# Performance work log

Measured on AMD Instinct MI355X. Metric: run time of the kernel, lower is better.

Reference implementation:

```python
import jax, jax.numpy as jnp
import numpy as np

EPS_BN = 1e-5
EPS_NORM = 1e-12
NUM_HEADS = 8


def _bn_relu(x):
    # BatchNorm2d in training mode with fresh params (gamma=1, beta=0), then ReLU.
    m = x.mean((0, 2, 3), keepdims=True)
    v = x.var((0, 2, 3), keepdims=True)  # biased variance, as PyTorch uses for normalization
    return jax.nn.relu((x - m) * jax.lax.rsqrt(v + EPS_BN))


def _conv3(x, w, groups=1):
    # 3x3 conv, stride 1, padding 1 (NCHW / OIHW)
    return jax.lax.conv_general_dilated(
        x, w, (1, 1), ((1, 1), (1, 1)),
        dimension_numbers=('NCHW', 'OIHW', 'NCHW'),
        feature_group_count=groups)


def _encoder(x, w1, w2, w3):
    # Conv1x1 -> BN -> ReLU -> Conv k2 s2 -> BN -> ReLU -> Conv1x1 -> BN -> ReLU
    x = _bn_relu(jnp.einsum('bihw,oi->bohw', x, w1))
    b, c, h, w = x.shape
    # k=2,s=2 conv as a reshape + einsum (non-overlapping 2x2 patches)
    x = _bn_relu(jnp.einsum('bchpwq,ocpq->bohw', x.reshape(b, c, h // 2, 2, w // 2, 2), w2))
    return _bn_relu(jnp.einsum('bihw,oi->bohw', x, w3))


def _decoder(x, w1, w2, w3):
    # ConvT1x1 -> BN -> ReLU -> ConvT k2 s2 -> BN -> ReLU -> ConvT1x1 -> BN -> ReLU
    x = _bn_relu(jnp.einsum('bihw,io->bohw', x, w1))
    # ConvTranspose k=2,s=2: each input pixel expands to a 2x2 block
    y = jnp.einsum('bihw,iopq->bohpwq', x, w2)
    b, o, h, p, w, q = y.shape
    x = _bn_relu(y.reshape(b, o, h * p, w * q))
    return _bn_relu(jnp.einsum('bihw,io->bohw', x, w3))


def _l2norm(x):
    # F.normalize(dim=-1) with eps=1e-12
    return x / jnp.maximum(jnp.linalg.norm(x, axis=-1, keepdims=True), EPS_NORM)


def setup_inputs() -> dict:
    key = jax.random.key(0)
    ks = jax.random.split(key, 13)
    B, C, H, W = 8, 256, 64, 64
    d = C // 4  # attention dim after self.divide

    def rn(k, shape, s=0.1):
        return jax.random.normal(k, shape, jnp.float32) * s

    return {
        'x': jax.random.normal(ks[0], (B, C, H, W), jnp.float32),
        'y': jax.random.normal(ks[1], (B, C, H, W), jnp.float32),
        'temperature': jnp.ones((NUM_HEADS, 1, 1), jnp.float32),
        'enc_w1': rn(ks[2], (d // 2, C)),
        'enc_w2': rn(ks[3], (d // 2, d // 2, 2, 2)),
        'enc_w3': rn(ks[4], (d, d // 2)),
        'kv_w': rn(ks[5], (2 * d, d)),
        'kv_dw_w': rn(ks[6], (2 * d, 1, 3, 3)),
        'q_w': rn(ks[7], (d, d)),
        'q_dw_w': rn(ks[8], (d, d, 3, 3)),
        'proj_w': rn(ks[9], (d, d)),
        'dec_w1': rn(ks[10], (d, 2 * d)),
        'dec_w2': rn(ks[11], (2 * d, 2 * d, 2, 2)),
        'dec_w3': rn(ks[12], (2 * d, 4 * d)),
    }


def reference(x, y, temperature, enc_w1, enc_w2, enc_w3, kv_w, kv_dw_w,
              q_w, q_dw_w, proj_w, dec_w1, dec_w2, dec_w3):
    # Shared freshly-built encoder applied to both x and y (same weights,
    # BN batch stats computed per call).
    x = _encoder(x, enc_w1, enc_w2, enc_w3)
    y = _encoder(y, enc_w1, enc_w2, enc_w3)
    b, c, h, w = x.shape  # c = 64, h = w = 32

    kv = _conv3(jnp.einsum('bihw,oi->bohw', x, kv_w), kv_dw_w, groups=2 * c)
    k, v = jnp.split(kv, 2, axis=1)
    q = _conv3(jnp.einsum('bihw,oi->bohw', y, q_w), q_dw_w)  # regular 3x3 conv

    ch = c // NUM_HEADS
    heads = lambda t: t.reshape(b, NUM_HEADS, ch, h * w)  # b head c (h w)
    q, k, v = heads(q), heads(k), heads(v)
    q = _l2norm(q)
    k = _l2norm(k)
    temp = temperature[None]  # [1, head, 1, 1]

    # Spatial attention: [b, head, hw, hw]
    attn_s = jax.nn.softmax(jnp.einsum('bhcn,bhcm->bhnm', q, k) * temp, axis=-1)
    out_s = jnp.einsum('bhcn,bhnm->bhcm', v, attn_s).reshape(b, c, h, w)
    out_s = jnp.einsum('bihw,oi->bohw', out_s, proj_w)

    # Channel attention: [b, head, c, c]
    attn_c = jax.nn.softmax(jnp.einsum('bhcn,bhdn->bhcd', q, k) * temp, axis=-1)
    out_c = jnp.einsum('bhcd,bhdn->bhcn', attn_c, v).reshape(b, c, h, w)
    out_c = jnp.einsum('bihw,oi->bohw', out_c, proj_w)

    return _decoder(out_s + out_c, dec_w1, dec_w2, dec_w3)
```

## Files before the change

### kernel.cpp

```cpp
#include <hip/hip_runtime.h>
#include <hip/hip_bf16.h>

#define EPS_BN 1e-5f

__global__ __launch_bounds__(256) void conv1x1_enc1_kernel(
    const float* __restrict__ in0, const float* __restrict__ in1,
    const float* __restrict__ w, float* __restrict__ out,
    float* __restrict__ stOut)
{
  __shared__ float il[2][32*64];
  __shared__ float wt[2][32*34];
  int tid  = threadIdx.x;
  int tile = blockIdx.x;
  int z    = blockIdx.y;
  int t    = z >> 3;
  const float* in  = t ? in1 : in0;
  const float* inb = in + ((size_t)(z&7))*256*4096 + tile*64;
  int cg = tid & 15;
  int og = tid >> 4;

  float4 vr[2]; float wr[4];
  int chA = tid >> 4;
  int chB = 16 + chA;
  int wo  = tid >> 5;
  int wch = tid & 31;

  vr[0] = *(const float4*)(inb + (size_t)chA*4096 + cg*4);
  vr[1] = *(const float4*)(inb + (size_t)chB*4096 + cg*4);
#pragma unroll
  for(int u=0;u<4;u++) wr[u] = w[(size_t)(wo+u*8)*256 + wch];
  ((float4*)il[0])[tid]     = vr[0];
  ((float4*)il[0])[tid+256] = vr[1];
#pragma unroll
  for(int u=0;u<4;u++) wt[0][wch*34 + wo + u*8] = wr[u];
  __syncthreads();

  float acc[2][4];
#pragma unroll
  for(int j=0;j<2;j++){ acc[j][0]=acc[j][1]=acc[j][2]=acc[j][3]=0.f; }

  for(int c=0;c<8;c++){
    int cur = c & 1;
    if(c < 7){
      int k0 = (c+1)*32;
      vr[0] = *(const float4*)(inb + (size_t)(k0+chA)*4096 + cg*4);
      vr[1] = *(const float4*)(inb + (size_t)(k0+chB)*4096 + cg*4);
#pragma unroll
      for(int u=0;u<4;u++) wr[u] = w[(size_t)(wo+u*8)*256 + k0 + wch];
    }
    const float4* ilc = (const float4*)il[cur];
    const float*  wtc = wt[cur];
#pragma unroll 8
    for(int ch=0; ch<32; ch++){
      float4 v  = ilc[ch*16 + cg];
      float2 wv = *(const float2*)&wtc[ch*34 + og*2];
      acc[0][0]=fmaf(wv.x,v.x,acc[0][0]); acc[0][1]=fmaf(wv.x,v.y,acc[0][1]);
      acc[0][2]=fmaf(wv.x,v.z,acc[0][2]); acc[0][3]=fmaf(wv.x,v.w,acc[0][3]);
      acc[1][0]=fmaf(wv.y,v.x,acc[1][0]); acc[1][1]=fmaf(wv.y,v.y,acc[1][1]);
      acc[1][2]=fmaf(wv.y,v.z,acc[1][2]); acc[1][3]=fmaf(wv.y,v.w,acc[1][3]);
    }
    if(c < 7){
      int nxt = 1 - cur;
      ((float4*)il[nxt])[tid]     = vr[0];
      ((float4*)il[nxt])[tid+256] = vr[1];
#pragma unroll
      for(int u=0;u<4;u++) wt[nxt][wch*34 + wo + u*8] = wr[u];
      __syncthreads();
    }
  }

  float* ob = out + ((size_t)z*32 + og*2)*4096 + tile*64 + cg*4;
#pragma unroll
  for(int j=0;j<2;j++){
    float4 vv = {acc[j][0],acc[j][1],acc[j][2],acc[j][3]};
    *(float4*)(ob + (size_t)j*4096) = vv;
  }
#pragma unroll
  for(int j=0;j<2;j++){
    float s  = acc[j][0]+acc[j][1]+acc[j][2]+acc[j][3];
    float s2 = acc[j][0]*acc[j][0]+acc[j][1]*acc[j][1]
             + acc[j][2]*acc[j][2]+acc[j][3]*acc[j][3];
    for(int off=8; off>0; off>>=1){
      s  += __shfl_down(s,  off, 16);
      s2 += __shfl_down(s2, off, 16);
    }
    if(cg==0){
      atomicAdd(&stOut[((size_t)t*32 + og*2 + j)*2],   s);
      atomicAdd(&stOut[((size_t)t*32 + og*2 + j)*2+1], s2);
    }
  }
}

template<int OT, bool HASBN, bool HASSTATS>
__global__ __launch_bounds__(256) void conv1x1_kernel(
    const float* __restrict__ in0, const float* __restrict__ in1,
    const float* __restrict__ w, float* __restrict__ out,
    const float* __restrict__ stIn, float* __restrict__ stOut,
    int I, int O, int P, int wio, int zsplit, float invN)
{
  __shared__ float wl[2048];
  __shared__ float bnm[256], bnr[256];
  int tid = threadIdx.x;
  int o0 = blockIdx.y*OT;
  int z  = blockIdx.z;
  int t  = (z >= zsplit) ? 1 : 0;
  int b  = t ? (z - zsplit) : z;
  const float* in = t ? in1 : in0;

  for(int idx=tid; idx<I*OT; idx+=256){
    int i = idx/OT, j = idx - i*OT;
    wl[idx] = wio ? w[(size_t)i*O + o0 + j] : w[(size_t)(o0+j)*I + i];
  }
  if(HASBN){
    for(int i=tid; i<I; i+=256){
      float s  = stIn[((size_t)t*I + i)*2];
      float s2 = stIn[((size_t)t*I + i)*2+1];
      float m  = s*invN;
      bnm[i] = m;
      bnr[i] = rsqrtf(s2*invN - m*m + EPS_BN);
    }
  }
  __syncthreads();

  int p4 = blockIdx.x*256 + tid;
  const float4* inb = (const float4*)(in + (size_t)b*I*P) + p4;
  int P4 = P >> 2;

  float acc[OT][4];
#pragma unroll
  for(int j=0;j<OT;j++){ acc[j][0]=acc[j][1]=acc[j][2]=acc[j][3]=0.f; }

  float4 vb[8];
  for(int i0=0;i0<I;i0+=8){
#pragma unroll
    for(int u=0;u<8;u++) vb[u] = inb[(size_t)(i0+u)*P4];
#pragma unroll
    for(int u=0;u<8;u++){
      float4 v = vb[u];
      if(HASBN){
        float m = bnm[i0+u], r = bnr[i0+u];
        v.x = fmaxf((v.x-m)*r, 0.f); v.y = fmaxf((v.y-m)*r, 0.f);
        v.z = fmaxf((v.z-m)*r, 0.f); v.w = fmaxf((v.w-m)*r, 0.f);
      }
      const float* wr = &wl[(i0+u)*OT];
#pragma unroll
      for(int j=0;j<OT;j++){
        float wv = wr[j];
        acc[j][0] = fmaf(wv, v.x, acc[j][0]);
        acc[j][1] = fmaf(wv, v.y, acc[j][1]);
        acc[j][2] = fmaf(wv, v.z, acc[j][2]);
        acc[j][3] = fmaf(wv, v.w, acc[j][3]);
      }
    }
  }

  float4* ob = (float4*)(out + ((size_t)z*O + o0)*P) + p4;
#pragma unroll
  for(int j=0;j<OT;j++){
    float4 vv = {acc[j][0], acc[j][1], acc[j][2], acc[j][3]};
    ob[(size_t)j*P4] = vv;
  }

  if(HASSTATS){
#pragma unroll
    for(int j=0;j<OT;j++){
      float s  = acc[j][0]+acc[j][1]+acc[j][2]+acc[j][3];
      float s2 = acc[j][0]*acc[j][0]+acc[j][1]*acc[j][1]
               + acc[j][2]*acc[j][2]+acc[j][3]*acc[j][3];
      for(int off=32; off>0; off>>=1){
        s  += __shfl_down(s,  off, 64);
        s2 += __shfl_down(s2, off, 64);
      }
      if((tid & 63)==0){
        atomicAdd(&stOut[((size_t)t*O + o0 + j)*2],   s);
        atomicAdd(&stOut[((size_t)t*O + o0 + j)*2+1], s2);
      }
    }
  }
}

template<int OT, bool HASBN, bool HASSTATS>
__global__ __launch_bounds__(256) void conv1x1_small(
    const float* __restrict__ in0, const float* __restrict__ in1,
    const float* __restrict__ w, float* __restrict__ out,
    const float* __restrict__ stIn, float* __restrict__ stOut,
    int I, int O, int wio, int zsplit, float invN)
{
  __shared__ float wl[512];
  __shared__ float bnm[128], bnr[128];
  int tid = threadIdx.x;
  int z  = blockIdx.z;
  int t  = (z >= zsplit) ? 1 : 0;
  int b  = t ? (z - zsplit) : z;
  const float* in = t ? in1 : in0;
  int W2 = 2*OT;

  for(int idx=tid; idx<I*W2; idx+=256){
    int i = idx/W2, slot = idx - i*W2;
    int oabs = blockIdx.y*W2 + slot;
    wl[idx] = wio ? w[(size_t)i*O + oabs] : w[(size_t)oabs*I + i];
  }
  if(HASBN){
    for(int i=tid; i<I; i+=256){
      float s  = stIn[((size_t)t*I + i)*2];
      float s2 = stIn[((size_t)t*I + i)*2+1];
      float m  = s*invN;
      bnm[i] = m;
      bnr[i] = rsqrtf(s2*invN - m*m + EPS_BN);
    }
  }
  __syncthreads();

  int p4 = blockIdx.x*128 + (tid & 127);
  int os = tid >> 7;
  const float4* inb = (const float4*)(in + (size_t)b*I*1024) + p4;

  float acc[OT][4];
#pragma unroll
  for(int j=0;j<OT;j++){ acc[j][0]=acc[j][1]=acc[j][2]=acc[j][3]=0.f; }

  float4 vb[8];
  for(int i0=0;i0<I;i0+=8){
#pragma unroll
    for(int u=0;u<8;u++) vb[u] = inb[(size_t)(i0+u)*256];
#pragma unroll
    for(int u=0;u<8;u++){
      float4 v = vb[u];
      if(HASBN){
        float m = bnm[i0+u], r = bnr[i0+u];
        v.x = fmaxf((v.x-m)*r, 0.f); v.y = fmaxf((v.y-m)*r, 0.f);
        v.z = fmaxf((v.z-m)*r, 0.f); v.w = fmaxf((v.w-m)*r, 0.f);
      }
      const float* wr = &wl[(i0+u)*W2 + os*OT];
#pragma unroll
      for(int j=0;j<OT;j++){
        float wv = wr[j];
        acc[j][0] = fmaf(wv, v.x, acc[j][0]);
        acc[j][1] = fmaf(wv, v.y, acc[j][1]);
        acc[j][2] = fmaf(wv, v.z, acc[j][2]);
        acc[j][3] = fmaf(wv, v.w, acc[j][3]);
      }
    }
  }

  int obase = blockIdx.y*W2 + os*OT;
  float4* ob = (float4*)(out + ((size_t)z*O + obase)*1024) + p4;
#pragma unroll
  for(int j=0;j<OT;j++){
    float4 vv = {acc[j][0], acc[j][1], acc[j][2], acc[j][3]};
    ob[(size_t)j*256] = vv;
  }

  if(HASSTATS){
#pragma unroll
    for(int j=0;j<OT;j++){
      float s  = acc[j][0]+acc[j][1]+acc[j][2]+acc[j][3];
      float s2 = acc[j][0]*acc[j][0]+acc[j][1]*acc[j][1]
               + acc[j][2]*acc[j][2]+acc[j][3]*acc[j][3];
      for(int off=32; off>0; off>>=1){
        s  += __shfl_down(s,  off, 64);
        s2 += __shfl_down(s2, off, 64);
      }
      if((tid & 63)==0){
        atomicAdd(&stOut[((size_t)t*O + obase + j)*2],   s);
        atomicAdd(&stOut[((size_t)t*O + obase + j)*2+1], s2);
      }
    }
  }
}

__global__ __launch_bounds__(256) void conv2x2s2_bn_kernel(
    const float* __restrict__ in, const float* __restrict__ w,
    float* __restrict__ out, const float* __restrict__ stIn,
    float* __restrict__ stOut, float invN)
{
  __shared__ float wl[512];
  __shared__ float bnm[32], bnr[32];
  int tid = threadIdx.x;
  int o0 = blockIdx.x*4;
  int rq = blockIdx.y;
  int z  = blockIdx.z;
  int t  = z >> 3;

  for(int idx=tid; idx<512; idx+=256){
    int osub = idx>>7, ch=(idx>>2)&31, pq=idx&3;
    wl[idx] = w[(((size_t)(o0+osub)*32 + ch)*4) + pq];
  }
  if(tid < 32){
    float s  = stIn[((size_t)t*32 + tid)*2];
    float s2 = stIn[((size_t)t*32 + tid)*2+1];
    float m  = s*invN;
    bnm[tid] = m;
    bnr[tid] = rsqrtf(s2*invN - m*m + EPS_BN);
  }
  __syncthreads();

  int os   = tid >> 6;
  int slot = tid & 63;
  int h    = rq*8 + (slot>>3);
  int wg   = slot & 7;
  int cb   = wg*8;
  const float* wbase = &wl[os*128];
  const float* inz = in + (size_t)z*32*4096;

  float acc[4] = {0,0,0,0};
  float4 c0,c1,c2,c3, n0_,n1_,n2_,n3_;
  c0 = *(const float4*)(inz + (size_t)0*4096 + (2*h)*64 + cb);
  c1 = *(const float4*)(inz + (size_t)0*4096 + (2*h)*64 + cb + 4);
  c2 = *(const float4*)(inz + (size_t)0*4096 + (2*h+1)*64 + cb);
  c3 = *(const float4*)(inz + (size_t)0*4096 + (2*h+1)*64 + cb + 4);
  for(int ch=0; ch<32; ch++){
    if(ch < 31){
      n0_ = *(const float4*)(inz + (size_t)(ch+1)*4096 + (2*h)*64 + cb);
      n1_ = *(const float4*)(inz + (size_t)(ch+1)*4096 + (2*h)*64 + cb + 4);
      n2_ = *(const float4*)(inz + (size_t)(ch+1)*4096 + (2*h+1)*64 + cb);
      n3_ = *(const float4*)(inz + (size_t)(ch+1)*4096 + (2*h+1)*64 + cb + 4);
    }
    float m = bnm[ch], r = bnr[ch];
    float t0[8] = {c0.x,c0.y,c0.z,c0.w,c1.x,c1.y,c1.z,c1.w};
    float t1[8] = {c2.x,c2.y,c2.z,c2.w,c3.x,c3.y,c3.z,c3.w};
#pragma unroll
    for(int e=0;e<8;e++){
      t0[e] = fmaxf((t0[e]-m)*r, 0.f);
      t1[e] = fmaxf((t1[e]-m)*r, 0.f);
    }
    const float* wp = wbase + ch*4;
#pragma unroll
    for(int k=0;k<4;k++){
      acc[k] = fmaf(wp[0], t0[2*k],   acc[k]);
      acc[k] = fmaf(wp[1], t0[2*k+1], acc[k]);
      acc[k] = fmaf(wp[2], t1[2*k],   acc[k]);
      acc[k] = fmaf(wp[3], t1[2*k+1], acc[k]);
    }
    c0=n0_; c1=n1_; c2=n2_; c3=n3_;
  }

  float4 vv = {acc[0],acc[1],acc[2],acc[3]};
  *(float4*)(out + ((size_t)z*32 + o0+os)*1024 + h*32 + wg*4) = vv;

  float s  = acc[0]+acc[1]+acc[2]+acc[3];
  float s2 = acc[0]*acc[0]+acc[1]*acc[1]+acc[2]*acc[2]+acc[3]*acc[3];
  for(int off=32; off>0; off>>=1){
    s  += __shfl_down(s,  off, 64);
    s2 += __shfl_down(s2, off, 64);
  }
  if((tid & 63)==0){
    atomicAdd(&stOut[((size_t)t*32 + o0 + os)*2],   s);
    atomicAdd(&stOut[((size_t)t*32 + o0 + os)*2+1], s2);
  }
}

__global__ __launch_bounds__(256) void upsample2x2_bn_kernel(
    const float* __restrict__ in, const float* __restrict__ w,
    float* __restrict__ out, const float* __restrict__ stIn,
    float* __restrict__ stOut, float invN)
{
  __shared__ float wl[1024];
  __shared__ float bnm[128], bnr[128];
  int tid = threadIdx.x;
  int o0 = blockIdx.x*2;
  int b  = blockIdx.y;

  for(int idx=tid; idx<1024; idx+=256){
    int pq = idx & 3, r = idx >> 2;
    int i = r >> 1, j = r & 1;
    wl[idx] = w[((size_t)i*128 + o0+j)*4 + pq];
  }
  if(tid < 128){
    float s  = stIn[(size_t)tid*2];
    float s2 = stIn[(size_t)tid*2+1];
    float m  = s*invN;
    bnm[tid] = m;
    bnr[tid] = rsqrtf(s2*invN - m*m + EPS_BN);
  }
  __syncthreads();

  int h  = tid >> 3;
  int wg = tid & 7;
  int w0 = wg*4;

  float acc[2][16];
#pragma unroll
  for(int j=0;j<2;j++) for(int e=0;e<16;e++) acc[j][e]=0.f;

  float4 vb4[8];
  for(int i0=0;i0<128;i0+=8){
#pragma unroll
    for(int u=0;u<8;u++)
      vb4[u] = *(const float4*)(in + (((size_t)b*128+i0+u)*1024) + h*32 + w0);
#pragma unroll
    for(int u=0;u<8;u++){
      int i = i0+u;
      float4 v = vb4[u];
      float m = bnm[i], r = bnr[i];
      float vk[4] = {fmaxf((v.x-m)*r,0.f), fmaxf((v.y-m)*r,0.f),
                     fmaxf((v.z-m)*r,0.f), fmaxf((v.w-m)*r,0.f)};
#pragma unroll
      for(int j=0;j<2;j++){
        const float* wj = &wl[(i*2+j)*4];
#pragma unroll
        for(int pq=0;pq<4;pq++){
#pragma unroll
          for(int k=0;k<4;k++)
            acc[j][pq*4+k] = fmaf(wj[pq], vk[k], acc[j][pq*4+k]);
        }
      }
    }
  }

#pragma unroll
  for(int j=0;j<2;j++){
    float* ob = out + ((size_t)b*128 + o0+j)*4096;
#pragma unroll
    for(int p=0;p<2;p++){
      float4 A = {acc[j][(p*2+0)*4+0], acc[j][(p*2+1)*4+0],
                  acc[j][(p*2+0)*4+1], acc[j][(p*2+1)*4+1]};
      float4 B = {acc[j][(p*2+0)*4+2], acc[j][(p*2+1)*4+2],
                  acc[j][(p*2+0)*4+3], acc[j][(p*2+1)*4+3]};
      *(float4*)(ob + (2*h+p)*64 + 2*w0)     = A;
      *(float4*)(ob + (2*h+p)*64 + 2*w0 + 4) = B;
    }
  }

#pragma unroll
  for(int j=0;j<2;j++){
    float s=0.f, s2=0.f;
#pragma unroll
    for(int e=0;e<16;e++){ s += acc[j][e]; s2 += acc[j][e]*acc[j][e]; }
    for(int off=32; off>0; off>>=1){
      s  += __shfl_down(s,  off, 64);
      s2 += __shfl_down(s2, off, 64);
    }
    if((tid & 63)==0){
      atomicAdd(&stOut[((size_t)(o0+j))*2],   s);
      atomicAdd(&stOut[((size_t)(o0+j))*2+1], s2);
    }
  }
}

__global__ __launch_bounds__(256) void bn_final_kernel(
    float* __restrict__ x, const float* __restrict__ st, float invN)
{
  int idx4 = blockIdx.x*256 + threadIdx.x;
  int c = (idx4 >> 10) & 255;
  float s  = st[(size_t)c*2];
  float s2 = st[(size_t)c*2+1];
  float m  = s*invN;
  float r  = rsqrtf(s2*invN - m*m + EPS_BN);
  float4 v = ((float4*)x)[idx4];
  v.x = fmaxf((v.x-m)*r, 0.f); v.y = fmaxf((v.y-m)*r, 0.f);
  v.z = fmaxf((v.z-m)*r, 0.f); v.w = fmaxf((v.w-m)*r, 0.f);
  ((float4*)x)[idx4] = v;
}

__global__ __launch_bounds__(256) void dwconv3x3_kernel(
    const float* __restrict__ in, const float* __restrict__ w,
    float* __restrict__ out, int C, int H, int Wd)
{
  int idx = blockIdx.x*256 + threadIdx.x;
  int c = blockIdx.y, b = blockIdx.z;
  if(idx >= H*Wd) return;
  int h = idx / Wd, x = idx - h*Wd;
  const float* inp = in + ((size_t)b*C + c)*H*Wd;
  float acc = 0.f;
#pragma unroll
  for(int p=0;p<3;p++){
    int hh = h + p - 1;
    if((unsigned)hh >= (unsigned)H) continue;
#pragma unroll
    for(int q=0;q<3;q++){
      int wv = x + q - 1;
      if((unsigned)wv >= (unsigned)Wd) continue;
      acc += w[c*9 + p*3 + q] * inp[hh*Wd + wv];
    }
  }
  out[((size_t)b*C + c)*H*Wd + idx] = acc;
}

__global__ __launch_bounds__(256) void conv3x3_kernel(
    const float* __restrict__ in, const float* __restrict__ w,
    float* __restrict__ out, int IC, int H, int Wd)
{
  int o = blockIdx.y, b = blockIdx.z;
  __shared__ float wl[576];
  for(int t=threadIdx.x; t<IC*9; t+=256) wl[t] = w[(size_t)o*IC*9 + t];
  __syncthreads();
  int idx = blockIdx.x*256 + threadIdx.x;
  if(idx >= H*Wd) return;
  int h = idx / Wd, x = idx - h*Wd;
  const float* inb = in + (size_t)b*IC*H*Wd;
  float acc = 0.f;
  for(int i=0;i<IC;i++){
    const float* inp = inb + (size_t)i*H*Wd;
    const float* wp  = wl + i*9;
#pragma unroll
    for(int p=0;p<3;p++){
      int hh = h + p - 1;
      if((unsigned)hh >= (unsigned)H) continue;
      const float* row = inp + hh*Wd;
#pragma unroll
      for(int q=0;q<3;q++){
        int wv = x + q - 1;
        if((unsigned)wv >= (unsigned)Wd) continue;
        acc = fmaf(wp[p*3+q], row[wv], acc);
      }
    }
  }
  out[((size_t)b*gridDim.y + o)*H*Wd + idx] = acc;
}

__global__ __launch_bounds__(256) void l2norm_kernel(
    float* __restrict__ q, float* __restrict__ kv)
{
  int r = blockIdx.x;
  float* p;
  if(r < 512){ int b=r>>6, c=r&63; p = q + ((size_t)b*64+c)*1024; }
  else { int rr=r-512; int b=rr>>6, c=rr&63; p = kv + ((size_t)b*128+c)*1024; }
  int tid = threadIdx.x;
  float4 v = ((float4*)p)[tid];
  float s = v.x*v.x + v.y*v.y + v.z*v.z + v.w*v.w;
  __shared__ float ls[256];
  ls[tid]=s; __syncthreads();
  for(int st=128; st>0; st>>=1){ if(tid<st) ls[tid]+=ls[tid+st]; __syncthreads(); }
  float scale = 1.f / fmaxf(sqrtf(ls[0]), 1e-12f);
  v.x*=scale; v.y*=scale; v.z*=scale; v.w*=scale;
  ((float4*)p)[tid] = v;
}

__global__ __launch_bounds__(256) void attn_pass1(
    const float* __restrict__ q, const float* __restrict__ kv,
    const float* __restrict__ temp, float* __restrict__ den_out)
{
  int bx = blockIdx.x, hh = blockIdx.y, b = blockIdx.z;
  int nchunk = bx >> 2, mq = bx & 3;
  int tid = threadIdx.x;
  __shared__ __align__(16) float kl[256*12];
  const float* kb = kv + ((size_t)b*128 + hh*8)*1024 + mq*256;
  for(int t=tid;t<2048;t+=256){ int c=t>>8, m=t&255; kl[m*12+c]=kb[(size_t)c*1024+m]; }
  __syncthreads();
  int n = nchunk*256 + tid;
  const float* qp = q + ((size_t)b*64 + hh*8)*1024 + n;
  float th = temp[hh];
  float mxb = fabsf(th);
  float qr[8];
#pragma unroll
  for(int c=0;c<8;c++) qr[c]=qp[(size_t)c*1024]*th;
  const float4* kl4 = (const float4*)kl;
  float den = 0.f, den2 = 0.f;
  for(int m=0;m<256;m+=2){
    float4 a  = kl4[m*3],     a2 = kl4[m*3+1];
    float4 bt = kl4[(m+1)*3], b2 = kl4[(m+1)*3+1];
    float s0 = qr[0]*a.x+qr[1]*a.y+qr[2]*a.z+qr[3]*a.w
             + qr[4]*a2.x+qr[5]*a2.y+qr[6]*a2.z+qr[7]*a2.w;
    float s1 = qr[0]*bt.x+qr[1]*bt.y+qr[2]*bt.z+qr[3]*bt.w
             + qr[4]*b2.x+qr[5]*b2.y+qr[6]*b2.z+qr[7]*b2.w;
    den  += __expf(s0 - mxb);
    den2 += __expf(s1 - mxb);
  }
  atomicAdd(&den_out[((size_t)(b*8+hh))*1024+n], den+den2);
}

__global__ __launch_bounds__(256) void attn_pass2(
    const float* __restrict__ q, const float* __restrict__ kv,
    const float* __restrict__ temp, const float* __restrict__ den,
    float* __restrict__ out)
{
  int bx = blockIdx.x, hh = blockIdx.y, b = blockIdx.z;
  int mchunk = bx >> 2, nq = bx & 3;
  int tid = threadIdx.x;
  __shared__ __align__(16) float ql[256*12];
  __shared__ __align__(16) float vl[256*12];
  __shared__ float idl[256];
  int bh = b*8+hh;
  int n0 = nq*256;
  const float* qb = q  + ((size_t)b*64 + hh*8)*1024 + n0;
  const float* vb = kv + ((size_t)b*128 + 64 + hh*8)*1024 + n0;
  for(int t=tid;t<2048;t+=256){
    int c=t>>8, n=t&255;
    ql[n*12+c] = qb[(size_t)c*1024+n];
    vl[n*12+c] = vb[(size_t)c*1024+n];
  }
  idl[tid] = 1.f/den[(size_t)bh*1024 + n0 + tid];
  __syncthreads();
  int m = mchunk*256 + tid;
  const float* kb = kv + ((size_t)b*128 + hh*8)*1024 + m;
  float th = temp[hh];
  float mxb = fabsf(th);
  float kr[8];
#pragma unroll
  for(int c=0;c<8;c++) kr[c]=kb[(size_t)c*1024]*th;
  float acc[8] = {0,0,0,0,0,0,0,0};
  const float4* ql4 = (const float4*)ql;
  const float4* vl4 = (const float4*)vl;
  for(int n=0;n<256;n+=2){
    float4 qa = ql4[n*3],     qa2 = ql4[n*3+1];
    float4 qc = ql4[(n+1)*3], qc2 = ql4[(n+1)*3+1];
    float s0 = kr[0]*qa.x+kr[1]*qa.y+kr[2]*qa.z+kr[3]*qa.w
             + kr[4]*qa2.x+kr[5]*qa2.y+kr[6]*qa2.z+kr[7]*qa2.w;
    float s1 = kr[0]*qc.x+kr[1]*qc.y+kr[2]*qc.z+kr[3]*qc.w
             + kr[4]*qc2.x+kr[5]*qc2.y+kr[6]*qc2.z+kr[7]*qc2.w;
    float p0 = __expf(s0 - mxb) * idl[n];
    float p1 = __expf(s1 - mxb) * idl[n+1];
    float4 va = vl4[n*3],     va2 = vl4[n*3+1];
    float4 vc = vl4[(n+1)*3], vc2 = vl4[(n+1)*3+1];
    acc[0]+=p0*va.x + p1*vc.x; acc[1]+=p0*va.y + p1*vc.y;
    acc[2]+=p0*va.z + p1*vc.z; acc[3]+=p0*va.w + p1*vc.w;
    acc[4]+=p0*va2.x + p1*vc2.x; acc[5]+=p0*va2.y + p1*vc2.y;
    acc[6]+=p0*va2.z + p1*vc2.z; acc[7]+=p0*va2.w + p1*vc2.w;
  }
  float* ob = out + ((size_t)b*64 + hh*8)*1024 + m;
#pragma unroll
  for(int c=0;c<8;c++) atomicAdd(&ob[(size_t)c*1024], acc[c]);
}

__global__ __launch_bounds__(256) void attn_channel(
    const float* __restrict__ q, const float* __restrict__ kv,
    const float* __restrict__ temp, float* out)
{
  int hh = blockIdx.x, b = blockIdx.y;
  __shared__ float kl[8192];
  const float* qb = q  + ((size_t)b*64 + hh*8)*1024;
  const float* kb = kv + ((size_t)b*128 + hh*8)*1024;
  const float* vb = kv + ((size_t)b*128 + 64 + hh*8)*1024;
  int tid = threadIdx.x;
  for(int t=tid;t<8192;t+=256) kl[t]=kb[t];
  __syncthreads();
  __shared__ float part[256];
  __shared__ float a[64];
  {
    int pair = tid >> 2, seg = tid & 3;
    int c = pair >> 3, d = pair & 7;
    const float* qrow = qb + (size_t)c*1024 + seg*256;
    const float* krow = kl + d*1024 + seg*256;
    float s = 0.f;
#pragma unroll 4
    for(int n=0;n<256;n++) s += qrow[n]*krow[n];
    part[tid] = s;
  }
  __syncthreads();
  if(tid < 64){
    float g = part[tid*4]+part[tid*4+1]+part[tid*4+2]+part[tid*4+3];
    part[tid] = g * temp[hh];
  }
  __syncthreads();
  if(tid < 8){
    float mx = -3.4e38f;
    for(int d=0;d<8;d++) mx = fmaxf(mx, part[tid*8+d]);
    float den = 0.f;
    float e[8];
    for(int d=0;d<8;d++){ e[d] = __expf(part[tid*8+d]-mx); den+=e[d]; }
    float inv = 1.f/den;
    for(int d=0;d<8;d++) a[tid*8+d] = e[d]*inv;
  }
  __syncthreads();
  float* ob = out + ((size_t)b*64 + hh*8)*1024;
  for(int n=tid;n<1024;n+=256){
    float vv[8];
#pragma unroll
    for(int d=0;d<8;d++) vv[d] = vb[(size_t)d*1024+n];
#pragma unroll
    for(int c=0;c<8;c++){
      float s = 0.f;
#pragma unroll
      for(int d=0;d<8;d++) s += a[c*8+d]*vv[d];
      ob[(size_t)c*1024+n] += s;
    }
  }
}

extern "C" void kernel_launch(void* const* d_in, const int* in_sizes, int n_in,
                              void* d_out, int out_size, void* d_ws, size_t ws_size,
                              hipStream_t stream)
{
  (void)in_sizes; (void)n_in; (void)out_size; (void)ws_size;
  const float* x      = (const float*)d_in[0];
  const float* y      = (const float*)d_in[1];
  const float* temp   = (const float*)d_in[2];
  const float* enc_w1 = (const float*)d_in[3];
  const float* enc_w2 = (const float*)d_in[4];
  const float* enc_w3 = (const float*)d_in[5];
  const float* kv_w   = (const float*)d_in[6];
  const float* kv_dw_w= (const float*)d_in[7];
  const float* q_w    = (const float*)d_in[8];
  const float* q_dw_w = (const float*)d_in[9];
  const float* proj_w = (const float*)d_in[10];
  const float* dec_w1 = (const float*)d_in[11];
  const float* dec_w2 = (const float*)d_in[12];
  const float* dec_w3 = (const float*)d_in[13];
  float* out = (float*)d_out;

  float* W   = (float*)d_ws;
  float* ST  = W;
  float* ST0 = ST;
  float* ST1 = ST + 128;
  float* ST2 = ST + 256;
  float* ST3 = ST + 512;
  float* ST4 = ST + 768;
  float* ST5 = ST + 1024;
  float* A    = W + 2048;
  float* E1   = A;
  float* KV1  = A;
  float* QPre = A + 1048576;
  float* ATTN = A;
  float* PROJ = A + 524288;
  float* D1   = A + 1048576;
  float* E2   = W + 2099200;
  float* E3   = W + 2623488;
  float* KV   = W + 3672064;
  float* Q    = W + 4720640;
  float* DEN  = W + 5244928;
  float* D2   = W + 2099200;

  const float inv32k = 1.f/32768.f, inv8k = 1.f/8192.f;

  hipMemsetAsync(ST, 0, 2048*sizeof(float), stream);
  hipMemsetAsync(DEN, 0, 65536*sizeof(float), stream);

  conv1x1_enc1_kernel<<<dim3(64,16),256,0,stream>>>(x, y, enc_w1, E1, ST0);
  conv2x2s2_bn_kernel<<<dim3(8,4,16),256,0,stream>>>(E1, enc_w2, E2, ST0, ST1, inv32k);
  conv1x1_small<1,true,true><<<dim3(2,32,16),256,0,stream>>>(
      E2, E2 + (size_t)8*32*1024, enc_w3, E3, ST1, ST2, 32, 64, 0, 8, inv8k);

  conv1x1_small<1,true,false><<<dim3(2,64,8),256,0,stream>>>(
      E3, E3, kv_w, KV1, ST2, nullptr, 64, 128, 0, 999, inv8k);
  dwconv3x3_kernel<<<dim3(4,128,8),256,0,stream>>>(KV1, kv_dw_w, KV, 128, 32, 32);
  conv1x1_small<1,true,false><<<dim3(2,32,8),256,0,stream>>>(
      E3 + (size_t)8*64*1024, E3, q_w, QPre, ST2 + 128, nullptr, 64, 64, 0, 999, inv8k);
  conv3x3_kernel<<<dim3(4,64,8),256,0,stream>>>(QPre, q_dw_w, Q, 64, 32, 32);

  hipMemsetAsync(ATTN, 0, 524288*sizeof(float), stream);

  l2norm_kernel<<<1024,256,0,stream>>>(Q, KV);

  attn_pass1<<<dim3(16,8,8),256,0,stream>>>(Q, KV, temp, DEN);
  attn_pass2<<<dim3(16,8,8),256,0,stream>>>(Q, KV, temp, DEN, ATTN);
  attn_channel<<<dim3(8,8),256,0,stream>>>(Q, KV, temp, ATTN);

  conv1x1_small<1,false,false><<<dim3(2,32,8),256,0,stream>>>(
      ATTN, ATTN, proj_w, PROJ, nullptr, nullptr, 64, 64, 0, 999, 0.f);

  conv1x1_small<1,false,true><<<dim3(2,64,8),256,0,stream>>>(
      PROJ, PROJ, dec_w1, D1, nullptr, ST3, 64, 128, 1, 999, 0.f);
  upsample2x2_bn_kernel<<<dim3(64,8),256,0,stream>>>(D1, dec_w2, D2, ST3, ST4, inv8k);
  conv1x1_kernel<8,true,true><<<dim3(4,32,8),256,0,stream>>>(
      D2, D2, dec_w3, out, ST4, ST5, 128, 256, 4096, 1, 999, inv32k);
  bn_final_kernel<<<8192,256,0,stream>>>(out, ST5, inv32k);
}
```

Baseline: 620.8 us.

## Vectorize 3x3 convs, defer L2 normalization into attention kernels, cap enc1 occupancy

The depthwise and full 3x3 conv kernels now compute four adjacent outputs per thread, using float4 row loads plus halo scalars in a 32x32 tile. This cuts redundant loads and index arithmetic. The l2norm kernel no longer rewrites Q and K in place. It only stores per-row inverse norms, which the attention kernels apply as they load data, saving one full read-modify-write pass. The enc1 conv also gets a launch-bounds minimum of two blocks per CU, which may constrain registers.

Measured after the change: 606.4 us. -2.3%, faster.

```diff
diff --git a/kernel.cpp b/kernel.cpp
--- a/kernel.cpp
+++ b/kernel.cpp
@@ -3,7 +3,7 @@
 
 #define EPS_BN 1e-5f
 
-__global__ __launch_bounds__(256) void conv1x1_enc1_kernel(
+__global__ __launch_bounds__(256,2) void conv1x1_enc1_kernel(
     const float* __restrict__ in0, const float* __restrict__ in1,
     const float* __restrict__ w, float* __restrict__ out,
     float* __restrict__ stOut)
@@ -455,88 +455,102 @@
 
 __global__ __launch_bounds__(256) void dwconv3x3_kernel(
     const float* __restrict__ in, const float* __restrict__ w,
-    float* __restrict__ out, int C, int H, int Wd)
-{
-  int idx = blockIdx.x*256 + threadIdx.x;
-  int c = blockIdx.y, b = blockIdx.z;
-  if(idx >= H*Wd) return;
-  int h = idx / Wd, x = idx - h*Wd;
-  const float* inp = in + ((size_t)b*C + c)*H*Wd;
-  float acc = 0.f;
-#pragma unroll
-  for(int p=0;p<3;p++){
-    int hh = h + p - 1;
-    if((unsigned)hh >= (unsigned)H) continue;
-#pragma unroll
-    for(int q=0;q<3;q++){
-      int wv = x + q - 1;
-      if((unsigned)wv >= (unsigned)Wd) continue;
-      acc += w[c*9 + p*3 + q] * inp[hh*Wd + wv];
-    }
-  }
-  out[((size_t)b*C + c)*H*Wd + idx] = acc;
+    float* __restrict__ out, int C)
+{
+  int c = blockIdx.x, b = blockIdx.y;
+  int tid = threadIdx.x;
+  __shared__ float wl[9];
+  if(tid < 9) wl[tid] = w[c*9 + tid];
+  __syncthreads();
+  int h = tid >> 3, x4 = tid & 7;
+  int c0 = x4*4;
+  const float* base = in + ((size_t)b*C + c)*1024;
+  float ax=0.f, ay=0.f, az=0.f, aw=0.f;
+#pragma unroll
+  for(int dr=0; dr<3; dr++){
+    int r = h + dr - 1;
+    if((unsigned)r >= 32u) continue;
+    const float* row = base + r*32 + c0;
+    float4 cc = *(const float4*)row;
+    float l  = (x4>0) ? row[-1] : 0.f;
+    float rr = (x4<7) ? row[4]  : 0.f;
+    float w0=wl[dr*3], w1=wl[dr*3+1], w2=wl[dr*3+2];
+    ax = fmaf(w0,l,   fmaf(w1,cc.x, fmaf(w2,cc.y, ax)));
+    ay = fmaf(w0,cc.x,fmaf(w1,cc.y, fmaf(w2,cc.z, ay)));
+    az = fmaf(w0,cc.y,fmaf(w1,cc.z, fmaf(w2,cc.w, az)));
+    aw = fmaf(w0,cc.z,fmaf(w1,cc.w, fmaf(w2,rr,  aw)));
+  }
+  float4 vv = {ax,ay,az,aw};
+  *(float4*)(out + ((size_t)b*C + c)*1024 + h*32 + c0) = vv;
 }
 
 __global__ __launch_bounds__(256) void conv3x3_kernel(
     const float* __restrict__ in, const float* __restrict__ w,
-    float* __restrict__ out, int IC, int H, int Wd)
-{
-  int o = blockIdx.y, b = blockIdx.z;
+    float* __restrict__ out, int IC)
+{
+  int o = blockIdx.x, b = blockIdx.y;
+  int tid = threadIdx.x;
   __shared__ float wl[576];
-  for(int t=threadIdx.x; t<IC*9; t+=256) wl[t] = w[(size_t)o*IC*9 + t];
-  __syncthreads();
-  int idx = blockIdx.x*256 + threadIdx.x;
-  if(idx >= H*Wd) return;
-  int h = idx / Wd, x = idx - h*Wd;
-  const float* inb = in + (size_t)b*IC*H*Wd;
-  float acc = 0.f;
+  for(int t=tid; t<IC*9; t+=256) wl[t] = w[(size_t)o*IC*9 + t];
+  __syncthreads();
+  int h = tid >> 3, x4 = tid & 7;
+  int c0 = x4*4;
+  const float* inb = in + (size_t)b*IC*1024;
+  float ax=0.f, ay=0.f, az=0.f, aw=0.f;
+#pragma unroll 2
   for(int i=0;i<IC;i++){
-    const float* inp = inb + (size_t)i*H*Wd;
-    const float* wp  = wl + i*9;
-#pragma unroll
-    for(int p=0;p<3;p++){
-      int hh = h + p - 1;
-      if((unsigned)hh >= (unsigned)H) continue;
-      const float* row = inp + hh*Wd;
-#pragma unroll
-      for(int q=0;q<3;q++){
-        int wv = x + q - 1;
-        if((unsigned)wv >= (unsigned)Wd) continue;
-        acc = fmaf(wp[p*3+q], row[wv], acc);
-      }
-    }
-  }
-  out[((size_t)b*gridDim.y + o)*H*Wd + idx] = acc;
-}
-
-__global__ __launch_bounds__(256) void l2norm_kernel(
-    float* __restrict__ q, float* __restrict__ kv)
+    const float* base = inb + (size_t)i*1024;
+    const float* wp = &wl[i*9];
+#pragma unroll
+    for(int dr=0; dr<3; dr++){
+      int r = h + dr - 1;
+      if((unsigned)r >= 32u) continue;
+      const float* row = base + r*32 + c0;
+      float4 cc = *(const float4*)row;
+      float l  = (x4>0) ? row[-1] : 0.f;
+      float rr = (x4<7) ? row[4]  : 0.f;
+      float w0=wp[dr*3], w1=wp[dr*3+1], w2=wp[dr*3+2];
+      ax = fmaf(w0,l,   fmaf(w1,cc.x, fmaf(w2,cc.y, ax)));
+      ay = fmaf(w0,cc.x,fmaf(w1,cc.y, fmaf(w2,cc.z, ay)));
+      az = fmaf(w0,cc.y,fmaf(w1,cc.z, fmaf(w2,cc.w, az)));
+      aw = fmaf(w0,cc.z,fmaf(w1,cc.w, fmaf(w2,rr,  aw)));
+    }
+  }
+  float4 vv = {ax,ay,az,aw};
+  *(float4*)(out + ((size_t)b*gridDim.x + o)*1024 + h*32 + c0) = vv;
+}
+
+__global__ __launch_bounds__(256) void norm_scale_kernel(
+    const float* __restrict__ q, const float* __restrict__ kv,
+    float* __restrict__ scl)
 {
   int r = blockIdx.x;
-  float* p;
+  const float* p;
   if(r < 512){ int b=r>>6, c=r&63; p = q + ((size_t)b*64+c)*1024; }
   else { int rr=r-512; int b=rr>>6, c=rr&63; p = kv + ((size_t)b*128+c)*1024; }
   int tid = threadIdx.x;
-  float4 v = ((float4*)p)[tid];
+  float4 v = ((const float4*)p)[tid];
   float s = v.x*v.x + v.y*v.y + v.z*v.z + v.w*v.w;
   __shared__ float ls[256];
   ls[tid]=s; __syncthreads();
   for(int st=128; st>0; st>>=1){ if(tid<st) ls[tid]+=ls[tid+st]; __syncthreads(); }
-  float scale = 1.f / fmaxf(sqrtf(ls[0]), 1e-12f);
-  v.x*=scale; v.y*=scale; v.z*=scale; v.w*=scale;
-  ((float4*)p)[tid] = v;
+  if(tid==0) scl[r] = 1.f/fmaxf(sqrtf(ls[0]), 1e-12f);
 }
 
 __global__ __launch_bounds__(256) void attn_pass1(
     const float* __restrict__ q, const float* __restrict__ kv,
-    const float* __restrict__ temp, float* __restrict__ den_out)
+    const float* __restrict__ temp, const float* __restrict__ scl,
+    float* __restrict__ den_out)
 {
   int bx = blockIdx.x, hh = blockIdx.y, b = blockIdx.z;
   int nchunk = bx >> 2, mq = bx & 3;
   int tid = threadIdx.x;
   __shared__ __align__(16) float kl[256*12];
   const float* kb = kv + ((size_t)b*128 + hh*8)*1024 + mq*256;
-  for(int t=tid;t<2048;t+=256){ int c=t>>8, m=t&255; kl[m*12+c]=kb[(size_t)c*1024+m]; }
+  for(int t=tid;t<2048;t+=256){
+    int c=t>>8, m=t&255;
+    kl[m*12+c] = kb[(size_t)c*1024+m] * scl[512 + b*64 + hh*8 + c];
+  }
   __syncthreads();
   int n = nchunk*256 + tid;
   const float* qp = q + ((size_t)b*64 + hh*8)*1024 + n;
@@ -544,7 +558,7 @@
   float mxb = fabsf(th);
   float qr[8];
 #pragma unroll
-  for(int c=0;c<8;c++) qr[c]=qp[(size_t)c*1024]*th;
+  for(int c=0;c<8;c++) qr[c] = qp[(size_t)c*1024] * scl[b*64+hh*8+c] * th;
   const float4* kl4 = (const float4*)kl;
   float den = 0.f, den2 = 0.f;
   for(int m=0;m<256;m+=2){
@@ -562,8 +576,8 @@
 
 __global__ __launch_bounds__(256) void attn_pass2(
     const float* __restrict__ q, const float* __restrict__ kv,
-    const float* __restrict__ temp, const float* __restrict__ den,
-    float* __restrict__ out)
+    const float* __restrict__ temp, const float* __restrict__ scl,
+    const float* __restrict__ den, float* __restrict__ out)
 {
   int bx = blockIdx.x, hh = blockIdx.y, b = blockIdx.z;
   int mchunk = bx >> 2, nq = bx & 3;
@@ -577,7 +591,7 @@
   const float* vb = kv + ((size_t)b*128 + 64 + hh*8)*1024 + n0;
   for(int t=tid;t<2048;t+=256){
     int c=t>>8, n=t&255;
-    ql[n*12+c] = qb[(size_t)c*1024+n];
+    ql[n*12+c] = qb[(size_t)c*1024+n] * scl[b*64+hh*8+c];
     vl[n*12+c] = vb[(size_t)c*1024+n];
   }
   idl[tid] = 1.f/den[(size_t)bh*1024 + n0 + tid];
@@ -588,7 +602,7 @@
   float mxb = fabsf(th);
   float kr[8];
 #pragma unroll
-  for(int c=0;c<8;c++) kr[c]=kb[(size_t)c*1024]*th;
+  for(int c=0;c<8;c++) kr[c] = kb[(size_t)c*1024] * scl[512+b*64+hh*8+c] * th;
   float acc[8] = {0,0,0,0,0,0,0,0};
   const float4* ql4 = (const float4*)ql;
   const float4* vl4 = (const float4*)vl;
@@ -615,7 +629,8 @@
 
 __global__ __launch_bounds__(256) void attn_channel(
     const float* __restrict__ q, const float* __restrict__ kv,
-    const float* __restrict__ temp, float* out)
+    const float* __restrict__ temp, const float* __restrict__ scl,
+    float* out)
 {
   int hh = blockIdx.x, b = blockIdx.y;
   __shared__ float kl[8192];
@@ -639,8 +654,9 @@
   }
   __syncthreads();
   if(tid < 64){
+    int c = tid >> 3, d = tid & 7;
     float g = part[tid*4]+part[tid*4+1]+part[tid*4+2]+part[tid*4+3];
-    part[tid] = g * temp[hh];
+    part[tid] = g * scl[b*64+hh*8+c] * scl[512+b*64+hh*8+d] * temp[hh];
   }
   __syncthreads();
   if(tid < 8){
@@ -708,7 +724,8 @@
   float* E3   = W + 2623488;
   float* KV   = W + 3672064;
   float* Q    = W + 4720640;
-  float* DEN  = W + 5244928;
+  float* SCL  = W + 5244928;
+  float* DEN  = W + 5245952;
   float* D2   = W + 2099200;
 
   const float inv32k = 1.f/32768.f, inv8k = 1.f/8192.f;
@@ -723,18 +740,18 @@
 
   conv1x1_small<1,true,false><<<dim3(2,64,8),256,0,stream>>>(
       E3, E3, kv_w, KV1, ST2, nullptr, 64, 128, 0, 999, inv8k);
-  dwconv3x3_kernel<<<dim3(4,128,8),256,0,stream>>>(KV1, kv_dw_w, KV, 128, 32, 32);
+  dwconv3x3_kernel<<<dim3(128,8),256,0,stream>>>(KV1, kv_dw_w, KV, 128);
   conv1x1_small<1,true,false><<<dim3(2,32,8),256,0,stream>>>(
       E3 + (size_t)8*64*1024, E3, q_w, QPre, ST2 + 128, nullptr, 64, 64, 0, 999, inv8k);
-  conv3x3_kernel<<<dim3(4,64,8),256,0,stream>>>(QPre, q_dw_w, Q, 64, 32, 32);
+  conv3x3_kernel<<<dim3(64,8),256,0,stream>>>(QPre, q_dw_w, Q, 64);
 
   hipMemsetAsync(ATTN, 0, 524288*sizeof(float), stream);
 
-  l2norm_kernel<<<1024,256,0,stream>>>(Q, KV);
-
-  attn_pass1<<<dim3(16,8,8),256,0,stream>>>(Q, KV, temp, DEN);
-  attn_pass2<<<dim3(16,8,8),256,0,stream>>>(Q, KV, temp, DEN, ATTN);
-  attn_channel<<<dim3(8,8),256,0,stream>>>(Q, KV, temp, ATTN);
+  norm_scale_kernel<<<1024,256,0,stream>>>(Q, KV, SCL);
+
+  attn_pass1<<<dim3(16,8,8),256,0,stream>>>(Q, KV, temp, SCL, DEN);
+  attn_pass2<<<dim3(16,8,8),256,0,stream>>>(Q, KV, temp, SCL, DEN, ATTN);
+  attn_channel<<<dim3(8,8),256,0,stream>>>(Q, KV, temp, SCL, ATTN);
 
   conv1x1_small<1,false,false><<<dim3(2,32,8),256,0,stream>>>(
       ATTN, ATTN, proj_w, PROJ, nullptr, nullptr, 64, 64, 0, 999, 0.f);
```
